# Optimization experiments

Measured on AMD Instinct MI355X. Metric: run time of the kernel, lower is better.

The kernel has to match this reference:

```python
import jax, jax.numpy as jnp
import numpy as np

N_NODES = 100000
N_EDGES = 1600000
N_GRAPHS = 64
D = 128          # input_features == hidden_sf*model_dim == out_sf*output_channels
N_CLASSES = 10   # out_dim
N_LAYERS = 3


def setup_inputs() -> dict:
    key = jax.random.key(0)
    ks = jax.random.split(key, 8)
    x = jax.random.normal(ks[0], (N_NODES, D), dtype=jnp.float32)
    edge_index = jax.random.randint(ks[1], (2, N_EDGES), 0, N_NODES, dtype=jnp.int64)
    batch = jnp.sort(jax.random.randint(ks[2], (N_NODES,), 0, N_GRAPHS, dtype=jnp.int64))
    s = 1.0 / np.sqrt(D)
    # PyG GraphConv: out = lin_rel(aggr(x_j)) + lin_root(x); lin_root has no bias
    W_rel = jax.random.uniform(ks[3], (N_LAYERS, D, D), jnp.float32, -s, s)
    W_root = jax.random.uniform(ks[4], (N_LAYERS, D, D), jnp.float32, -s, s)
    b_rel = jax.random.uniform(ks[5], (N_LAYERS, D), jnp.float32, -s, s)
    W_fc = jax.random.uniform(ks[6], (D, N_CLASSES), jnp.float32, -s, s)
    b_fc = jax.random.uniform(ks[7], (N_CLASSES,), jnp.float32, -s, s)
    return dict(x=x, edge_index=edge_index, batch=batch,
                W_rel=W_rel, W_root=W_root, b_rel=b_rel, W_fc=W_fc, b_fc=b_fc)


def reference(x, edge_index, batch, W_rel, W_root, b_rel, W_fc, b_fc):
    src, dst = edge_index[0], edge_index[1]  # messages flow src -> dst
    for i in range(N_LAYERS):  # small fixed layer count
        agg = jax.ops.segment_sum(x[src], dst, num_segments=N_NODES)  # [N, D] gather+scatter-add
        x = agg @ W_rel[i] + b_rel[i] + x @ W_root[i]
    # global mean pool over graphs
    counts = jax.ops.segment_sum(jnp.ones((N_NODES,), x.dtype), batch, num_segments=N_GRAPHS)
    pooled = jax.ops.segment_sum(x, batch, num_segments=N_GRAPHS) / jnp.maximum(counts, 1.0)[:, None]
    logits = pooled @ W_fc + b_fc  # [N_GRAPHS, N_CLASSES]
    return jax.nn.log_softmax(logits, axis=1)
```

## Files before the change

### kernel.cpp

```cpp
#include <hip/hip_runtime.h>
#include <hip/hip_bf16.h>

#define D 128
#define NGRAPHS 64
#define NCLASSES 10
#define NB 800
#define CAP 3072
#define EPB 8192

typedef unsigned short u16;
typedef unsigned int u32;
typedef __attribute__((ext_vector_type(8))) short bf16x8;
typedef __attribute__((ext_vector_type(4))) float f32x4;

__device__ __forceinline__ u16 rne_bf16(float f) {
  u32 u = __float_as_uint(f);
  u += 0x7FFFu + ((u >> 16) & 1u);
  return (u16)(u >> 16);
}
__device__ __forceinline__ float bf_lo(u32 u) { return __uint_as_float(u << 16); }
__device__ __forceinline__ float bf_hi(u32 u) { return __uint_as_float(u & 0xFFFF0000u); }

__global__ __launch_bounds__(256) void k_cast0(const float* __restrict__ x,
                                               u16* __restrict__ xb, long long n8) {
  long long i = (long long)blockIdx.x * 256 + threadIdx.x;
  if (i >= n8) return;
  const float4* xp = reinterpret_cast<const float4*>(x) + i * 2;
  float4 a = xp[0], b = xp[1];
  u32 w0 = rne_bf16(a.x) | ((u32)rne_bf16(a.y) << 16);
  u32 w1 = rne_bf16(a.z) | ((u32)rne_bf16(a.w) << 16);
  u32 w2 = rne_bf16(b.x) | ((u32)rne_bf16(b.y) << 16);
  u32 w3 = rne_bf16(b.z) | ((u32)rne_bf16(b.w) << 16);
  reinterpret_cast<uint4*>(xb)[i] = make_uint4(w0, w1, w2, w3);
}

__global__ __launch_bounds__(256) void k_prep_wt(const float* __restrict__ W_rel,
                                                 const float* __restrict__ W_root,
                                                 u16* __restrict__ Wt) {
  int id = blockIdx.x * 256 + threadIdx.x;
  if (id >= 6 * D * D) return;
  int col = id & 127;
  int k = (id >> 7) & 127;
  int m = id >> 14;
  const float* src = (m < 3) ? (W_rel + (size_t)m * D * D) : (W_root + (size_t)(m - 3) * D * D);
  Wt[(size_t)m * D * D + col * D + k] = rne_bf16(src[k * D + col]);
}

__global__ __launch_bounds__(256) void k_bin(
    const int* __restrict__ src, const int* __restrict__ dst,
    int* __restrict__ gcnt, u32* __restrict__ ebuf, int n_edges, int nb) {
  __shared__ int lh[NB];
  int tid = threadIdx.x;
  int e0 = blockIdx.x * EPB;
  for (int b = tid; b < NB; b += 256) lh[b] = 0;
  __syncthreads();
  for (int i = tid; i < EPB; i += 256) {
    int e = e0 + i;
    if (e < n_edges) atomicAdd(&lh[dst[e] >> 7], 1);
  }
  __syncthreads();
  for (int b = tid; b < nb; b += 256) {
    int c = lh[b];
    lh[b] = (c > 0) ? (b * CAP + atomicAdd(&gcnt[b], c)) : 0;
  }
  __syncthreads();
  for (int i = tid; i < EPB; i += 256) {
    int e = e0 + i;
    if (e < n_edges) {
      int d = dst[e];
      int slot = atomicAdd(&lh[d >> 7], 1);
      ebuf[slot] = ((u32)(d & 127) << 20) | (u32)src[e];
    }
  }
}

__global__ __launch_bounds__(256) void k_sort(
    const u32* __restrict__ ebuf, const int* __restrict__ gcnt,
    u32* __restrict__ eidx, int* __restrict__ rowptr, int* __restrict__ deg,
    int n_nodes) {
  __shared__ u32 earr[CAP];
  __shared__ int lh[128], sc[128], lcur[128];
  int tid = threadIdx.x;
  int b = blockIdx.x;
  int cnt = gcnt[b];
  int base = b * CAP;
  for (int i = tid; i < cnt; i += 256) earr[i] = ebuf[base + i];
  if (tid < 128) lh[tid] = 0;
  __syncthreads();
  for (int i = tid; i < cnt; i += 256) atomicAdd(&lh[earr[i] >> 20], 1);
  __syncthreads();
  if (tid < 128) sc[tid] = lh[tid];
  __syncthreads();
  #pragma unroll
  for (int off = 1; off < 128; off <<= 1) {
    int v = (tid < 128 && tid >= off) ? sc[tid - off] : 0;
    __syncthreads();
    if (tid < 128) sc[tid] += v;
    __syncthreads();
  }
  if (tid < 128) {
    int excl = sc[tid] - lh[tid];
    int n = b * 128 + tid;
    if (n < n_nodes) { rowptr[n] = base + excl; deg[n] = lh[tid]; }
    lcur[tid] = excl;
  }
  __syncthreads();
  for (int i = tid; i < cnt; i += 256) {
    u32 e = earr[i];
    int slot = atomicAdd(&lcur[e >> 20], 1);
    eidx[base + slot] = e & 0xFFFFF;
  }
}

__global__ __launch_bounds__(256) void k_gather(
    const u16* __restrict__ xb, const int* __restrict__ rowptr,
    const int* __restrict__ deg, const u32* __restrict__ eidx,
    u16* __restrict__ aggb, int n_nodes) {
  int tid = threadIdx.x;
  int n = blockIdx.x * 16 + (tid >> 4);
  int c = tid & 15;
  if (n >= n_nodes) return;
  int beg = rowptr[n];
  int dn = deg[n];
  float a0 = 0, a1 = 0, a2 = 0, a3 = 0, a4 = 0, a5 = 0, a6 = 0, a7 = 0;
  for (int i = 0; i < dn; i++) {
    int s = (int)eidx[beg + i];
    uint4 v = *(reinterpret_cast<const uint4*>(xb + (size_t)s * D) + c);
    a0 += bf_lo(v.x); a1 += bf_hi(v.x);
    a2 += bf_lo(v.y); a3 += bf_hi(v.y);
    a4 += bf_lo(v.z); a5 += bf_hi(v.z);
    a6 += bf_lo(v.w); a7 += bf_hi(v.w);
  }
  u32 w0 = rne_bf16(a0) | ((u32)rne_bf16(a1) << 16);
  u32 w1 = rne_bf16(a2) | ((u32)rne_bf16(a3) << 16);
  u32 w2 = rne_bf16(a4) | ((u32)rne_bf16(a5) << 16);
  u32 w3 = rne_bf16(a6) | ((u32)rne_bf16(a7) << 16);
  *(reinterpret_cast<uint4*>(aggb + (size_t)n * D) + c) = make_uint4(w0, w1, w2, w3);
}

__global__ __launch_bounds__(256) void k_gemm_mfma(
    const u16* __restrict__ A1, const u16* __restrict__ A2,
    const u16* __restrict__ Wt1, const u16* __restrict__ Wt2,
    const float* __restrict__ bias, u16* __restrict__ outp, int M) {
  __shared__ __align__(16) u16 As[128 * 64];
  __shared__ __align__(16) u16 Ws[128 * 64];
  int tid = threadIdx.x;
  int wave = tid >> 6, lane = tid & 63;
  int g = lane >> 4, lr = lane & 15;
  int r0 = blockIdx.x * 128;
  int wr = wave * 32;

  f32x4 acc[2][8];
  #pragma unroll
  for (int fr = 0; fr < 2; fr++)
    #pragma unroll
    for (int fc = 0; fc < 8; fc++)
      acc[fr][fc] = (f32x4){0.f, 0.f, 0.f, 0.f};

  int srow = tid >> 1;
  int shalf = tid & 1;

  #pragma unroll 1
  for (int pass = 0; pass < 2; pass++) {
    const u16* A = pass ? A2 : A1;
    const u16* Wt = pass ? Wt2 : Wt1;
    #pragma unroll 1
    for (int kh = 0; kh < 2; kh++) {
      int rg = r0 + srow; if (rg >= M) rg = M - 1;
      const u16* ga = A + (size_t)rg * D + kh * 64 + shalf * 32;
      const u16* gw = Wt + (size_t)srow * D + kh * 64 + shalf * 32;
      #pragma unroll
      for (int cch = 0; cch < 4; cch++) {
        int boff = ((shalf * 64 + cch * 16) ^ ((srow & 7) << 4)) >> 1;
        uint4 va = *reinterpret_cast<const uint4*>(ga + cch * 8);
        *reinterpret_cast<uint4*>(&As[srow * 64 + boff]) = va;
        uint4 vw = *reinterpret_cast<const uint4*>(gw + cch * 8);
        *reinterpret_cast<uint4*>(&Ws[srow * 64 + boff]) = vw;
      }
      __syncthreads();
      #pragma unroll
      for (int kc = 0; kc < 2; kc++) {
        int kbyte = kc * 64 + g * 16;
        bf16x8 af[2];
        #pragma unroll
        for (int fr = 0; fr < 2; fr++) {
          int row = wr + fr * 16 + lr;
          int ob = (kbyte ^ ((row & 7) << 4)) >> 1;
          af[fr] = *reinterpret_cast<const bf16x8*>(&As[row * 64 + ob]);
        }
        #pragma unroll
        for (int fc = 0; fc < 8; fc++) {
          int colw = fc * 16 + lr;
          int ob = (kbyte ^ ((colw & 7) << 4)) >> 1;
          bf16x8 bfv = *reinterpret_cast<const bf16x8*>(&Ws[colw * 64 + ob]);
          #pragma unroll
          for (int fr = 0; fr < 2; fr++)
            acc[fr][fc] = __builtin_amdgcn_mfma_f32_16x16x32_bf16(
                af[fr], bfv, acc[fr][fc], 0, 0, 0);
        }
      }
      __syncthreads();
    }
  }

  #pragma unroll
  for (int fc = 0; fc < 8; fc++) {
    float bc = bias[fc * 16 + lr];
    #pragma unroll
    for (int fr = 0; fr < 2; fr++) {
      #pragma unroll
      for (int j = 0; j < 4; j++) {
        int R = r0 + wr + fr * 16 + g * 4 + j;
        if (R < M)
          outp[(size_t)R * D + fc * 16 + lr] = rne_bf16(acc[fr][fc][j] + bc);
      }
    }
  }
}

#define CHUNK 256
__global__ __launch_bounds__(256) void k_pool(
    const u16* __restrict__ xb, const int* __restrict__ batch,
    float* __restrict__ pooled, int n_nodes) {
  int col = threadIdx.x & 127;
  int sub = threadIdx.x >> 7;
  int n0 = blockIdx.x * CHUNK;
  int nend = min(n0 + CHUNK, n_nodes);
  float sum = 0.f; int cur = -1;
  for (int n = n0 + sub; n < nend; n += 2) {
    int g = batch[n];
    if (g != cur) {
      if (cur >= 0) atomicAdd(&pooled[cur * D + col], sum);
      sum = 0.f; cur = g;
    }
    sum += __uint_as_float((u32)xb[(size_t)n * D + col] << 16);
  }
  if (cur >= 0) atomicAdd(&pooled[cur * D + col], sum);
}

__global__ __launch_bounds__(256) void k_bounds(
    const int* __restrict__ batch, int* __restrict__ start, int n) {
  int i = blockIdx.x * 256 + threadIdx.x;
  if (i >= n) return;
  int g = batch[i];
  if (i == 0 || batch[i - 1] != g) start[g] = i;
}

__global__ void k_head(const float* __restrict__ pooled, const int* __restrict__ gstart,
                       const float* __restrict__ W_fc, const float* __restrict__ b_fc,
                       float* __restrict__ outp, int n_nodes) {
  int g = threadIdx.x;
  if (g >= NGRAPHS) return;
  int s = gstart[g];
  int c = 0;
  if (s >= 0) {
    int e = n_nodes;
    for (int h = g + 1; h < NGRAPHS; h++)
      if (gstart[h] >= 0) { e = gstart[h]; break; }
    c = e - s;
  }
  float inv = 1.0f / fmaxf((float)c, 1.0f);
  float logits[NCLASSES];
  #pragma unroll
  for (int j = 0; j < NCLASSES; j++) logits[j] = b_fc[j];
  for (int k = 0; k < D; k++) {
    float p = pooled[g * D + k] * inv;
    #pragma unroll
    for (int j = 0; j < NCLASSES; j++) logits[j] += p * W_fc[k * NCLASSES + j];
  }
  float m = logits[0];
  #pragma unroll
  for (int j = 1; j < NCLASSES; j++) m = fmaxf(m, logits[j]);
  float s2 = 0.f;
  #pragma unroll
  for (int j = 0; j < NCLASSES; j++) s2 += expf(logits[j] - m);
  float lse = m + logf(s2);
  #pragma unroll
  for (int j = 0; j < NCLASSES; j++) outp[g * NCLASSES + j] = logits[j] - lse;
}

extern "C" void kernel_launch(void* const* d_in, const int* in_sizes, int n_in,
                              void* d_out, int out_size, void* d_ws, size_t ws_size,
                              hipStream_t stream) {
  const float* x      = (const float*)d_in[0];
  const int*   ei     = (const int*)d_in[1];
  const int*   batch  = (const int*)d_in[2];
  const float* W_rel  = (const float*)d_in[3];
  const float* W_root = (const float*)d_in[4];
  const float* b_rel  = (const float*)d_in[5];
  const float* W_fc   = (const float*)d_in[6];
  const float* b_fc   = (const float*)d_in[7];
  float* outp = (float*)d_out;

  int n_nodes = in_sizes[0] / D;
  int n_edges = in_sizes[1] / 2;
  const int* src = ei;
  const int* dst = ei + n_edges;
  int nb = (n_nodes + 127) / 128;

  char* ws = (char*)d_ws;
  size_t bb = (size_t)n_nodes * D * sizeof(u16);
  size_t nbts = (size_t)n_nodes * sizeof(int);
  u16* aggb   = (u16*)(ws);
  u16* xba    = (u16*)(ws + bb);
  u16* xbb    = (u16*)(ws + 2 * bb);
  char* p     = ws + 3 * bb;
  u16* Wt     = (u16*)(p);               p += (size_t)6 * D * D * sizeof(u16);
  int* gcnt   = (int*)(p);               p += (size_t)NB * sizeof(int);
  u32* ebuf   = (u32*)(p);               p += (size_t)NB * CAP * sizeof(u32);
  u32* eidx   = (u32*)(p);               p += (size_t)NB * CAP * sizeof(u32);
  int* rowptr = (int*)(p);               p += nbts;
  int* deg    = (int*)(p);               p += nbts;
  float* pooled = (float*)(p);           p += (size_t)NGRAPHS * D * sizeof(float);
  int* gstart = (int*)(p);

  k_prep_wt<<<(6 * D * D + 255) / 256, 256, 0, stream>>>(W_rel, W_root, Wt);
  long long n8 = (long long)n_nodes * D / 8;
  k_cast0<<<(int)((n8 + 255) / 256), 256, 0, stream>>>(x, xba, n8);
  hipMemsetAsync(gcnt, 0, (size_t)NB * sizeof(int), stream);
  k_bin<<<(n_edges + EPB - 1) / EPB, 256, 0, stream>>>(src, dst, gcnt, ebuf, n_edges, nb);
  k_sort<<<nb, 256, 0, stream>>>(ebuf, gcnt, eidx, rowptr, deg, n_nodes);

  u16* xc = xba;
  u16* xn = xbb;
  int gemmblk = (n_nodes + 127) / 128;
  for (int l = 0; l < 3; l++) {
    k_gather<<<(n_nodes + 15) / 16, 256, 0, stream>>>(xc, rowptr, deg, eidx, aggb, n_nodes);
    k_gemm_mfma<<<gemmblk, 256, 0, stream>>>(
        aggb, xc, Wt + (size_t)l * D * D, Wt + (size_t)(3 + l) * D * D,
        b_rel + (size_t)l * D, xn, n_nodes);
    u16* t = xc; xc = xn; xn = t;
  }

  hipMemsetAsync(pooled, 0, (size_t)NGRAPHS * D * sizeof(float), stream);
  hipMemsetAsync(gstart, 0xFF, (size_t)NGRAPHS * sizeof(int), stream);
  k_pool<<<(n_nodes + CHUNK - 1) / CHUNK, 256, 0, stream>>>(xc, batch, pooled, n_nodes);
  k_bounds<<<(n_nodes + 255) / 256, 256, 0, stream>>>(batch, gstart, n_nodes);
  k_head<<<1, 64, 0, stream>>>(pooled, gstart, W_fc, b_fc, outp, n_nodes);
}
```

Baseline: 547.8 us.

## Double-buffer GEMM tiles via direct global-to-LDS loads and unroll gather by four

The GEMM kernel now stages A and W tiles straight into LDS with global_load_lds, using two buffers so the next K-slice loads while MFMAs run on the current one. This removes the register round-trip and one barrier per stage. The gather kernel unrolls its edge loop by four so more independent row loads are in flight per thread. In exchange LDS use doubles, which can lower occupancy. The overlap also relies on correct wait/barrier ordering for the async LDS loads, since only one __syncthreads sits per stage.

```diff
diff --git a/kernel.cpp b/kernel.cpp
--- a/kernel.cpp
+++ b/kernel.cpp
@@ -20,6 +20,12 @@
 }
 __device__ __forceinline__ float bf_lo(u32 u) { return __uint_as_float(u << 16); }
 __device__ __forceinline__ float bf_hi(u32 u) { return __uint_as_float(u & 0xFFFF0000u); }
+
+__device__ __forceinline__ void gload_lds16(const void* g, void* l) {
+  __builtin_amdgcn_global_load_lds(
+      (const __attribute__((address_space(1))) void*)g,
+      (__attribute__((address_space(3))) void*)l, 16, 0, 0);
+}
 
 __global__ __launch_bounds__(256) void k_cast0(const float* __restrict__ x,
                                                u16* __restrict__ xb, long long n8) {
@@ -123,7 +129,26 @@
   int beg = rowptr[n];
   int dn = deg[n];
   float a0 = 0, a1 = 0, a2 = 0, a3 = 0, a4 = 0, a5 = 0, a6 = 0, a7 = 0;
-  for (int i = 0; i < dn; i++) {
+  int i = 0;
+  for (; i + 4 <= dn; i += 4) {
+    int s0 = (int)eidx[beg + i];
+    int s1 = (int)eidx[beg + i + 1];
+    int s2 = (int)eidx[beg + i + 2];
+    int s3 = (int)eidx[beg + i + 3];
+    uint4 v0 = *(reinterpret_cast<const uint4*>(xb + (size_t)s0 * D) + c);
+    uint4 v1 = *(reinterpret_cast<const uint4*>(xb + (size_t)s1 * D) + c);
+    uint4 v2 = *(reinterpret_cast<const uint4*>(xb + (size_t)s2 * D) + c);
+    uint4 v3 = *(reinterpret_cast<const uint4*>(xb + (size_t)s3 * D) + c);
+    a0 += bf_lo(v0.x) + bf_lo(v1.x) + bf_lo(v2.x) + bf_lo(v3.x);
+    a1 += bf_hi(v0.x) + bf_hi(v1.x) + bf_hi(v2.x) + bf_hi(v3.x);
+    a2 += bf_lo(v0.y) + bf_lo(v1.y) + bf_lo(v2.y) + bf_lo(v3.y);
+    a3 += bf_hi(v0.y) + bf_hi(v1.y) + bf_hi(v2.y) + bf_hi(v3.y);
+    a4 += bf_lo(v0.z) + bf_lo(v1.z) + bf_lo(v2.z) + bf_lo(v3.z);
+    a5 += bf_hi(v0.z) + bf_hi(v1.z) + bf_hi(v2.z) + bf_hi(v3.z);
+    a6 += bf_lo(v0.w) + bf_lo(v1.w) + bf_lo(v2.w) + bf_lo(v3.w);
+    a7 += bf_hi(v0.w) + bf_hi(v1.w) + bf_hi(v2.w) + bf_hi(v3.w);
+  }
+  for (; i < dn; i++) {
     int s = (int)eidx[beg + i];
     uint4 v = *(reinterpret_cast<const uint4*>(xb + (size_t)s * D) + c);
     a0 += bf_lo(v.x); a1 += bf_hi(v.x);
@@ -142,8 +167,8 @@
     const u16* __restrict__ A1, const u16* __restrict__ A2,
     const u16* __restrict__ Wt1, const u16* __restrict__ Wt2,
     const float* __restrict__ bias, u16* __restrict__ outp, int M) {
-  __shared__ __align__(16) u16 As[128 * 64];
-  __shared__ __align__(16) u16 Ws[128 * 64];
+  __shared__ __align__(16) u16 As[2][128 * 64];
+  __shared__ __align__(16) u16 Ws[2][128 * 64];
   int tid = threadIdx.x;
   int wave = tid >> 6, lane = tid & 63;
   int g = lane >> 4, lr = lane & 15;
@@ -157,50 +182,55 @@
     for (int fc = 0; fc < 8; fc++)
       acc[fr][fc] = (f32x4){0.f, 0.f, 0.f, 0.f};
 
-  int srow = tid >> 1;
-  int shalf = tid & 1;
+  const u16* Am[2] = {A1, A2};
+  const u16* Wm[2] = {Wt1, Wt2};
+
+  auto STAGE = [&](int buf, const u16* A, const u16* Wt, int kh) {
+    #pragma unroll
+    for (int i = 0; i < 4; i++) {
+      int gI = i * 256 + tid;
+      int row = gI >> 3;
+      int cs = (gI & 7) ^ (row & 7);
+      int rg = r0 + row; if (rg >= M) rg = M - 1;
+      u16* la = &As[buf][(size_t)(i * 256 + wave * 64) * 8];
+      gload_lds16(A + (size_t)rg * D + kh * 64 + cs * 8, la);
+      u16* lw = &Ws[buf][(size_t)(i * 256 + wave * 64) * 8];
+      gload_lds16(Wt + (size_t)row * D + kh * 64 + cs * 8, lw);
+    }
+  };
+
+  STAGE(0, A1, Wt1, 0);
+  __syncthreads();
 
   #pragma unroll 1
-  for (int pass = 0; pass < 2; pass++) {
-    const u16* A = pass ? A2 : A1;
-    const u16* Wt = pass ? Wt2 : Wt1;
-    #pragma unroll 1
-    for (int kh = 0; kh < 2; kh++) {
-      int rg = r0 + srow; if (rg >= M) rg = M - 1;
-      const u16* ga = A + (size_t)rg * D + kh * 64 + shalf * 32;
-      const u16* gw = Wt + (size_t)srow * D + kh * 64 + shalf * 32;
+  for (int s = 0; s < 4; s++) {
+    if (s < 3) {
+      int ns = s + 1;
+      STAGE(ns & 1, Am[ns >> 1], Wm[ns >> 1], ns & 1);
+    }
+    int buf = s & 1;
+    #pragma unroll
+    for (int kc = 0; kc < 2; kc++) {
+      int kbyte = kc * 64 + g * 16;
+      bf16x8 af[2];
       #pragma unroll
-      for (int cch = 0; cch < 4; cch++) {
-        int boff = ((shalf * 64 + cch * 16) ^ ((srow & 7) << 4)) >> 1;
-        uint4 va = *reinterpret_cast<const uint4*>(ga + cch * 8);
-        *reinterpret_cast<uint4*>(&As[srow * 64 + boff]) = va;
-        uint4 vw = *reinterpret_cast<const uint4*>(gw + cch * 8);
-        *reinterpret_cast<uint4*>(&Ws[srow * 64 + boff]) = vw;
+      for (int fr = 0; fr < 2; fr++) {
+        int row = wr + fr * 16 + lr;
+        int ob = (kbyte ^ ((row & 7) << 4)) >> 1;
+        af[fr] = *reinterpret_cast<const bf16x8*>(&As[buf][row * 64 + ob]);
       }
-      __syncthreads();
       #pragma unroll
-      for (int kc = 0; kc < 2; kc++) {
-        int kbyte = kc * 64 + g * 16;
-        bf16x8 af[2];
+      for (int fc = 0; fc < 8; fc++) {
+        int colw = fc * 16 + lr;
+        int ob = (kbyte ^ ((colw & 7) << 4)) >> 1;
+        bf16x8 bfv = *reinterpret_cast<const bf16x8*>(&Ws[buf][colw * 64 + ob]);
         #pragma unroll
-        for (int fr = 0; fr < 2; fr++) {
-          int row = wr + fr * 16 + lr;
-          int ob = (kbyte ^ ((row & 7) << 4)) >> 1;
-          af[fr] = *reinterpret_cast<const bf16x8*>(&As[row * 64 + ob]);
-        }
-        #pragma unroll
-        for (int fc = 0; fc < 8; fc++) {
-          int colw = fc * 16 + lr;
-          int ob = (kbyte ^ ((colw & 7) << 4)) >> 1;
-          bf16x8 bfv = *reinterpret_cast<const bf16x8*>(&Ws[colw * 64 + ob]);
-          #pragma unroll
-          for (int fr = 0; fr < 2; fr++)
-            acc[fr][fc] = __builtin_amdgcn_mfma_f32_16x16x32_bf16(
-                af[fr], bfv, acc[fr][fc], 0, 0, 0);
-        }
+        for (int fr = 0; fr < 2; fr++)
+          acc[fr][fc] = __builtin_amdgcn_mfma_f32_16x16x32_bf16(
+              af[fr], bfv, acc[fr][fc], 0, 0, 0);
       }
-      __syncthreads();
-    }
+    }
+    __syncthreads();
   }
 
   #pragma unroll
```

After: 497.4 us. 1.1x faster.
